# Kernel optimization log

Hardware: AMD Instinct MI355X
Metric: run time of the kernel (lower is better)

Reference implementation:

```python
import jax, jax.numpy as jnp
import numpy as np

N_GROUPS = 20000
K = 12
C_IN = 256
C_CH = 128
EPS = 1e-5


def _layernorm(x, g, b):
    mu = jnp.mean(x, axis=-1, keepdims=True)
    var = jnp.mean((x - mu) ** 2, axis=-1, keepdims=True)
    return (x - mu) * jax.lax.rsqrt(var + EPS) * g + b


def _linear(x, W, b):
    # torch nn.Linear: y = x @ W.T + b, W: [out, in]
    return x @ W.T + b


def setup_inputs() -> dict:
    key = jax.random.key(0)
    ks = jax.random.split(key, 16)
    nnz = N_GROUPS * K
    s_in = 1.0 / np.sqrt(C_IN)
    s_ch = 1.0 / np.sqrt(C_CH)
    return {
        "values": jax.random.normal(ks[0], (nnz, C_IN), jnp.float32),
        "ln_in_g": jnp.ones((C_IN,), jnp.float32),
        "ln_in_b": jnp.zeros((C_IN,), jnp.float32),
        "W_ga": jax.random.normal(ks[1], (C_CH, C_IN), jnp.float32) * s_in,
        "b_ga": jax.random.normal(ks[2], (C_CH,), jnp.float32) * 0.02,
        "W_la": jax.random.normal(ks[3], (C_CH, C_IN), jnp.float32) * s_in,
        "b_la": jnp.zeros((C_CH,), jnp.float32),
        "W_gb": jax.random.normal(ks[4], (C_CH, C_IN), jnp.float32) * s_in,
        "b_gb": jax.random.normal(ks[5], (C_CH,), jnp.float32) * 0.02,
        "W_lb": jax.random.normal(ks[6], (C_CH, C_IN), jnp.float32) * s_in,
        "b_lb": jnp.zeros((C_CH,), jnp.float32),
        "ln_o_g": jnp.ones((C_CH,), jnp.float32),
        "ln_o_b": jnp.zeros((C_CH,), jnp.float32),
        "W_go": jax.random.normal(ks[7], (C_IN, C_IN), jnp.float32) * s_in,
        "b_go": jax.random.normal(ks[8], (C_IN,), jnp.float32) * 0.02,
        "W_lo": jax.random.normal(ks[9], (C_IN, C_CH), jnp.float32) * s_ch,
        "b_lo": jax.random.normal(ks[10], (C_IN,), jnp.float32) * 0.02,
        "indices": jax.random.randint(ks[11], (4, nnz), 0, 20000, jnp.int64 if jax.config.jax_enable_x64 else jnp.int32),
    }


def reference(values, ln_in_g, ln_in_b, W_ga, b_ga, W_la, b_la, W_gb, b_gb,
              W_lb, b_lb, ln_o_g, ln_o_b, W_go, b_go, W_lo, b_lo, indices):
    nnz = values.shape[0]
    # input layer norm over channel dim of sparse values
    x = _layernorm(values, ln_in_g, ln_in_b)  # [nnz, C_IN]
    # gated projections to channel_dim
    a = jax.nn.sigmoid(_linear(x, W_ga, b_ga)) * _linear(x, W_la, b_la)  # [nnz, C_CH]
    b = jax.nn.sigmoid(_linear(x, W_gb, b_gb)) * _linear(x, W_lb, b_lb)
    a = a.reshape(nnz // K, K, C_CH)
    b = b.reshape(nnz // K, K, C_CH)
    # axis == 1: einsum('iko,jko->iko', a, b) = a * sum_j b[j]
    tri = a * jnp.sum(b, axis=0, keepdims=True)  # [nnz//K, K, C_CH]
    tri = tri.reshape(nnz, C_CH)
    # output: gate on x times linear of normed triangular update
    out = jax.nn.sigmoid(_linear(x, W_go, b_go)) * _linear(
        _layernorm(tri, ln_o_g, ln_o_b), W_lo, b_lo)  # [nnz, C_IN]
    return out
```

## Files before the change

kernel.cpp:

```cpp
#include <hip/hip_runtime.h>


#define NNZ   240000
#define ROWS  64
#define NBLK  (NNZ / ROWS)
#define PSLOTS 32

typedef __attribute__((ext_vector_type(8))) short bf16x8;
typedef __attribute__((ext_vector_type(4))) float f32x4;

__device__ __forceinline__ unsigned short f2bf(float f) {
  unsigned int u = __float_as_uint(f);
  u += 0x7fffu + ((u >> 16) & 1u);
  return (unsigned short)(u >> 16);
}
__device__ __forceinline__ float bf2f(unsigned short h) {
  return __uint_as_float(((unsigned int)h) << 16);
}

__global__ __launch_bounds__(256) void prep_kernel(
    const float* __restrict__ Wga, const float* __restrict__ Wla,
    const float* __restrict__ Wgb, const float* __restrict__ Wlb,
    const float* __restrict__ Wgo, const float* __restrict__ Wlo,
    unsigned short* __restrict__ wcat, unsigned short* __restrict__ wgo16,
    unsigned short* __restrict__ wlo16, float* __restrict__ bsum,
    float* __restrict__ bpart)
{
  const int tid = blockIdx.x * 256 + threadIdx.x;
  if (tid < 12 * 128) bsum[tid] = 0.f;
  if (tid < PSLOTS * 1536) bpart[tid] = 0.f;
  if (tid < 131072) {
    const int w8 = tid & 7, c = tid >> 3;
    const int m = c & 15, q = (c >> 4) & 3, t = (c >> 6) & 3;
    const int kb = (c >> 8) & 7, wv = c >> 11;
    const int k = kb * 32 + q * 8 + w8;
    const int ch = ((wv & 3) << 5) + ((t & 1) << 4) + m;
    const float* src = (wv < 4) ? (t < 2 ? Wga : Wla) : (t < 2 ? Wgb : Wlb);
    wcat[tid] = f2bf(src[ch * 256 + k]);
  } else if (tid < 196608) {
    const int o = tid - 131072;
    const int w8 = o & 7, c = o >> 3;
    const int m = c & 15, q = (c >> 4) & 3, nt = (c >> 6) & 1;
    const int kb = (c >> 7) & 7, wv = c >> 10;
    wgo16[o] = f2bf(Wgo[(wv * 32 + nt * 16 + m) * 256 + kb * 32 + q * 8 + w8]);
  } else if (tid < 229376) {
    const int o = tid - 196608;
    const int w8 = o & 7, c = o >> 3;
    const int m = c & 15, q = (c >> 4) & 3, nt = (c >> 6) & 1;
    const int kb = (c >> 7) & 3, wv = c >> 9;
    wlo16[o] = f2bf(Wlo[(wv * 32 + nt * 16 + m) * 128 + kb * 32 + q * 8 + w8]);
  }
}

__global__ __launch_bounds__(512, 4) void k1_kernel(
    const float* __restrict__ values,
    const float* __restrict__ ln_g, const float* __restrict__ ln_b,
    const float* __restrict__ b_ga, const float* __restrict__ b_la,
    const float* __restrict__ b_gb, const float* __restrict__ b_lb,
    const unsigned short* __restrict__ wcat,
    unsigned short* __restrict__ x_ws,
    unsigned short* __restrict__ a_ws,
    float* __restrict__ bpart)
{
  __shared__ unsigned short x_lds[ROWS][256];
  __shared__ float b_raw[ROWS][132];
  const int tid = threadIdx.x;
  const int rbase = blockIdx.x * ROWS;

  {
    const int r = tid >> 3, j = tid & 7;
    const size_t grow = (size_t)(rbase + r) * 256;
    float4 v[8];
    float s1 = 0.f, s2 = 0.f;
#pragma unroll
    for (int i = 0; i < 4; i++) {
      const int e = (j + 8 * i) * 8;
      const float4 t0 = *(const float4*)(values + grow + e);
      const float4 t1 = *(const float4*)(values + grow + e + 4);
      v[2 * i] = t0; v[2 * i + 1] = t1;
      s1 += t0.x + t0.y + t0.z + t0.w + t1.x + t1.y + t1.z + t1.w;
      s2 += t0.x * t0.x + t0.y * t0.y + t0.z * t0.z + t0.w * t0.w
          + t1.x * t1.x + t1.y * t1.y + t1.z * t1.z + t1.w * t1.w;
    }
    s1 += __shfl_xor(s1, 1); s1 += __shfl_xor(s1, 2); s1 += __shfl_xor(s1, 4);
    s2 += __shfl_xor(s2, 1); s2 += __shfl_xor(s2, 2); s2 += __shfl_xor(s2, 4);
    const float mu = s1 * (1.f / 256.f);
    const float rstd = rsqrtf(s2 * (1.f / 256.f) - mu * mu + 1e-5f);
    const int jp = j ^ (r & 7);
#pragma unroll
    for (int i = 0; i < 4; i++) {
      const int e = (j + 8 * i) * 8;
      const float4 a0 = v[2 * i], a1 = v[2 * i + 1];
      const float4 g0 = *(const float4*)(ln_g + e);
      const float4 g1 = *(const float4*)(ln_g + e + 4);
      const float4 c0 = *(const float4*)(ln_b + e);
      const float4 c1 = *(const float4*)(ln_b + e + 4);
      bf16x8 h;
      h[0] = (short)f2bf((a0.x - mu) * rstd * g0.x + c0.x);
      h[1] = (short)f2bf((a0.y - mu) * rstd * g0.y + c0.y);
      h[2] = (short)f2bf((a0.z - mu) * rstd * g0.z + c0.z);
      h[3] = (short)f2bf((a0.w - mu) * rstd * g0.w + c0.w);
      h[4] = (short)f2bf((a1.x - mu) * rstd * g1.x + c1.x);
      h[5] = (short)f2bf((a1.y - mu) * rstd * g1.y + c1.y);
      h[6] = (short)f2bf((a1.z - mu) * rstd * g1.z + c1.z);
      h[7] = (short)f2bf((a1.w - mu) * rstd * g1.w + c1.w);
      const int p = (jp + 8 * i) * 8;
      *(bf16x8*)(x_ws + grow + p) = h;
      *(bf16x8*)&x_lds[r][p] = h;
    }
  }
  __syncthreads();

  const int wv = tid >> 6;
  const int lane = tid & 63;
  const int m = lane & 15, q = lane >> 4;

  f32x4 acc[4][4];
#pragma unroll
  for (int a = 0; a < 4; a++)
#pragma unroll
    for (int b = 0; b < 4; b++) acc[a][b] = (f32x4){0.f, 0.f, 0.f, 0.f};

#pragma unroll
  for (int kb = 0; kb < 8; kb++) {
    bf16x8 A[4], B[4];
#pragma unroll
    for (int mt = 0; mt < 4; mt++)
      A[mt] = *(const bf16x8*)&x_lds[mt * 16 + m][((kb * 4 + q) ^ (m & 7)) << 3];
#pragma unroll
    for (int t = 0; t < 4; t++)
      B[t] = *(const bf16x8*)(wcat + ((((wv * 8 + kb) * 4 + t) * 64 + lane) << 3));
#pragma unroll
    for (int t = 0; t < 4; t++)
#pragma unroll
      for (int mt = 0; mt < 4; mt++)
        acc[mt][t] = __builtin_amdgcn_mfma_f32_16x16x32_bf16(A[mt], B[t], acc[mt][t], 0, 0, 0);
  }

  const bool isA = (wv < 4);
  const int chbase = (wv & 3) * 32;
  const float* bgp = isA ? b_ga : b_gb;
  const float* blp = isA ? b_la : b_lb;
#pragma unroll
  for (int t = 0; t < 2; t++) {
    const int ch = chbase + t * 16 + m;
    const float bgv = bgp[ch], blv = blp[ch];
#pragma unroll
    for (int mt = 0; mt < 4; mt++) {
#pragma unroll
      for (int rg = 0; rg < 4; rg++) {
        const int lrow = mt * 16 + q * 4 + rg;
        const float gv = acc[mt][t][rg] + bgv;
        const float lv = acc[mt][t + 2][rg] + blv;
        const float val = lv / (1.f + __expf(-gv));
        if (isA) {
          a_ws[(size_t)(rbase + lrow) * 128 + ch] = f2bf(val);
        } else {
          b_raw[lrow][ch] = val;
        }
      }
    }
  }
  __syncthreads();

  const int rb12 = rbase % 12;
  float* dst = bpart + (blockIdx.x & (PSLOTS - 1)) * 1536;
#pragma unroll
  for (int it = 0; it < 3; it++) {
    const int s = tid + it * 512;
    const int k12 = s >> 7, ch = s & 127;
    int r0 = k12 - rb12; if (r0 < 0) r0 += 12;
    float sum = 0.f;
    for (int r = r0; r < ROWS; r += 12) sum += b_raw[r][ch];
    atomicAdd(&dst[s], sum);
  }
}

__global__ __launch_bounds__(256) void reduce_kernel(
    const float* __restrict__ bpart, float* __restrict__ bsum)
{
  const int c = blockIdx.x * 256 + threadIdx.x;
  float s = 0.f;
#pragma unroll
  for (int sl = 0; sl < PSLOTS; sl++) s += bpart[sl * 1536 + c];
  bsum[c] = s;
}

__global__ __launch_bounds__(512, 4) void k2_kernel(
    const unsigned short* __restrict__ x_ws,
    const unsigned short* __restrict__ a_ws,
    const float* __restrict__ bsum,
    const float* __restrict__ ln_g, const float* __restrict__ ln_b,
    const unsigned short* __restrict__ wgo,
    const unsigned short* __restrict__ wlo,
    const float* __restrict__ b_go, const float* __restrict__ b_lo,
    float* __restrict__ out)
{
  __shared__ unsigned short x_lds[ROWS][256];
  __shared__ unsigned short t_lds[ROWS][128];
  const int tid = threadIdx.x;
  const int rbase = blockIdx.x * ROWS;

  {
    const bf16x8* xsrc = (const bf16x8*)(x_ws + (size_t)rbase * 256);
    bf16x8* xdst = (bf16x8*)&x_lds[0][0];
#pragma unroll
    for (int i = 0; i < 4; i++)
      xdst[tid + i * 512] = xsrc[tid + i * 512];

    const int r = tid >> 3, j = tid & 7;
    const int row = rbase + r;
    const int k12 = row % 12;
    const unsigned short* ar = a_ws + (size_t)row * 128;
    const float* bs = bsum + k12 * 128;
    float tv[16];
    float s1 = 0.f, s2 = 0.f;
#pragma unroll
    for (int i = 0; i < 2; i++) {
      const int e = (j + 8 * i) * 8;
      const ushort4 a0 = *(const ushort4*)(ar + e);
      const ushort4 a1 = *(const ushort4*)(ar + e + 4);
      const float4 b0 = *(const float4*)(bs + e);
      const float4 b1 = *(const float4*)(bs + e + 4);
      const float t0 = bf2f(a0.x) * b0.x, t1 = bf2f(a0.y) * b0.y;
      const float t2 = bf2f(a0.z) * b0.z, t3 = bf2f(a0.w) * b0.w;
      const float t4 = bf2f(a1.x) * b1.x, t5 = bf2f(a1.y) * b1.y;
      const float t6 = bf2f(a1.z) * b1.z, t7 = bf2f(a1.w) * b1.w;
      tv[8*i+0] = t0; tv[8*i+1] = t1; tv[8*i+2] = t2; tv[8*i+3] = t3;
      tv[8*i+4] = t4; tv[8*i+5] = t5; tv[8*i+6] = t6; tv[8*i+7] = t7;
      s1 += t0 + t1 + t2 + t3 + t4 + t5 + t6 + t7;
      s2 += t0*t0 + t1*t1 + t2*t2 + t3*t3 + t4*t4 + t5*t5 + t6*t6 + t7*t7;
    }
    s1 += __shfl_xor(s1, 1); s1 += __shfl_xor(s1, 2); s1 += __shfl_xor(s1, 4);
    s2 += __shfl_xor(s2, 1); s2 += __shfl_xor(s2, 2); s2 += __shfl_xor(s2, 4);
    const float mu = s1 * (1.f / 128.f);
    const float rstd = rsqrtf(s2 * (1.f / 128.f) - mu * mu + 1e-5f);
    const int jp = j ^ (r & 7);
#pragma unroll
    for (int i = 0; i < 2; i++) {
      const int e = (j + 8 * i) * 8;
      const float4 g0 = *(const float4*)(ln_g + e);
      const float4 g1 = *(const float4*)(ln_g + e + 4);
      const float4 c0 = *(const float4*)(ln_b + e);
      const float4 c1 = *(const float4*)(ln_b + e + 4);
      bf16x8 h;
      h[0] = (short)f2bf((tv[8*i+0] - mu) * rstd * g0.x + c0.x);
      h[1] = (short)f2bf((tv[8*i+1] - mu) * rstd * g0.y + c0.y);
      h[2] = (short)f2bf((tv[8*i+2] - mu) * rstd * g0.z + c0.z);
      h[3] = (short)f2bf((tv[8*i+3] - mu) * rstd * g0.w + c0.w);
      h[4] = (short)f2bf((tv[8*i+4] - mu) * rstd * g1.x + c1.x);
      h[5] = (short)f2bf((tv[8*i+5] - mu) * rstd * g1.y + c1.y);
      h[6] = (short)f2bf((tv[8*i+6] - mu) * rstd * g1.z + c1.z);
      h[7] = (short)f2bf((tv[8*i+7] - mu) * rstd * g1.w + c1.w);
      *(bf16x8*)&t_lds[r][(jp + 8 * i) * 8] = h;
    }
  }
  __syncthreads();

  const int wv = tid >> 6, lane = tid & 63;
  const int m = lane & 15, q = lane >> 4;

  f32x4 ag[4][2], al[4][2];
#pragma unroll
  for (int a = 0; a < 4; a++)
#pragma unroll
    for (int b = 0; b < 2; b++) { ag[a][b] = (f32x4){0.f,0.f,0.f,0.f}; al[a][b] = (f32x4){0.f,0.f,0.f,0.f}; }

#pragma unroll
  for (int kb = 0; kb < 8; kb++) {
    bf16x8 A[4], B[2];
#pragma unroll
    for (int mt = 0; mt < 4; mt++)
      A[mt] = *(const bf16x8*)&x_lds[mt * 16 + m][((kb * 4 + q) ^ (m & 7)) << 3];
#pragma unroll
    for (int nt = 0; nt < 2; nt++)
      B[nt] = *(const bf16x8*)(wgo + ((((wv * 8 + kb) * 2 + nt) * 64 + lane) << 3));
#pragma unroll
    for (int nt = 0; nt < 2; nt++)
#pragma unroll
      for (int mt = 0; mt < 4; mt++)
        ag[mt][nt] = __builtin_amdgcn_mfma_f32_16x16x32_bf16(A[mt], B[nt], ag[mt][nt], 0, 0, 0);
  }
#pragma unroll
  for (int kb = 0; kb < 4; kb++) {
    bf16x8 A[4], B[2];
#pragma unroll
    for (int mt = 0; mt < 4; mt++)
      A[mt] = *(const bf16x8*)&t_lds[mt * 16 + m][((kb * 4 + q) ^ (m & 7)) << 3];
#pragma unroll
    for (int nt = 0; nt < 2; nt++)
      B[nt] = *(const bf16x8*)(wlo + ((((wv * 4 + kb) * 2 + nt) * 64 + lane) << 3));
#pragma unroll
    for (int nt = 0; nt < 2; nt++)
#pragma unroll
      for (int mt = 0; mt < 4; mt++)
        al[mt][nt] = __builtin_amdgcn_mfma_f32_16x16x32_bf16(A[mt], B[nt], al[mt][nt], 0, 0, 0);
  }

#pragma unroll
  for (int nt = 0; nt < 2; nt++) {
    const int n = wv * 32 + nt * 16 + m;
    const float bgo = b_go[n], blo = b_lo[n];
#pragma unroll
    for (int mt = 0; mt < 4; mt++) {
#pragma unroll
      for (int rg = 0; rg < 4; rg++) {
        const int row = rbase + mt * 16 + q * 4 + rg;
        const float gv = ag[mt][nt][rg] + bgo;
        const float lv = al[mt][nt][rg] + blo;
        out[(size_t)row * 256 + n] = lv / (1.f + __expf(-gv));
      }
    }
  }
}

extern "C" void kernel_launch(void* const* d_in, const int* in_sizes, int n_in,
                              void* d_out, int out_size, void* d_ws, size_t ws_size,
                              hipStream_t stream) {
  (void)in_sizes; (void)n_in; (void)out_size; (void)ws_size;
  const float* values  = (const float*)d_in[0];
  const float* ln_in_g = (const float*)d_in[1];
  const float* ln_in_b = (const float*)d_in[2];
  const float* W_ga = (const float*)d_in[3];
  const float* b_ga = (const float*)d_in[4];
  const float* W_la = (const float*)d_in[5];
  const float* b_la = (const float*)d_in[6];
  const float* W_gb = (const float*)d_in[7];
  const float* b_gb = (const float*)d_in[8];
  const float* W_lb = (const float*)d_in[9];
  const float* b_lb = (const float*)d_in[10];
  const float* ln_o_g = (const float*)d_in[11];
  const float* ln_o_b = (const float*)d_in[12];
  const float* W_go = (const float*)d_in[13];
  const float* b_go = (const float*)d_in[14];
  const float* W_lo = (const float*)d_in[15];
  const float* b_lo = (const float*)d_in[16];

  char* ws = (char*)d_ws;
  unsigned short* x_ws  = (unsigned short*)(ws + 0);
  unsigned short* a_ws  = (unsigned short*)(ws + 122880000);
  unsigned short* wcat  = (unsigned short*)(ws + 184320000);
  unsigned short* wgo16 = (unsigned short*)(ws + 184582144);
  unsigned short* wlo16 = (unsigned short*)(ws + 184713216);
  float*          bsum  = (float*)        (ws + 184778752);
  float*          bpart = (float*)        (ws + 184784896);

  hipLaunchKernelGGL(prep_kernel, dim3(896), dim3(256), 0, stream,
                     W_ga, W_la, W_gb, W_lb, W_go, W_lo, wcat, wgo16, wlo16,
                     bsum, bpart);
  hipLaunchKernelGGL(k1_kernel, dim3(NBLK), dim3(512), 0, stream,
                     values, ln_in_g, ln_in_b, b_ga, b_la, b_gb, b_lb,
                     wcat, x_ws, a_ws, bpart);
  hipLaunchKernelGGL(reduce_kernel, dim3(6), dim3(256), 0, stream,
                     bpart, bsum);
  hipLaunchKernelGGL(k2_kernel, dim3(NBLK), dim3(512), 0, stream,
                     x_ws, a_ws, bsum, ln_o_g, ln_o_b, wgo16, wlo16, b_go, b_lo,
                     (float*)d_out);
}
```

Baseline: 627.7 us.

## Compute output gate in k1 and pass fp16 sigmoid to k2 instead of x

Moves the W_go gate GEMM and its sigmoid from k2 into k1, where the normalized x already sits in LDS. k1 writes the gate result as fp16 in an MFMA-fragment-native layout, so k2 no longer reloads x (256 bf16 per row) into LDS and only reads 256 fp16 gate values per row. k2 drops its x LDS buffer, which allows a higher occupancy hint. The gate is now stored at fp16 precision, and k1 gains extra register pressure and MFMA work.

```diff
diff --git a/kernel.cpp b/kernel.cpp
--- a/kernel.cpp
+++ b/kernel.cpp
@@ -8,6 +8,7 @@
 
 typedef __attribute__((ext_vector_type(8))) short bf16x8;
 typedef __attribute__((ext_vector_type(4))) float f32x4;
+typedef __attribute__((ext_vector_type(8))) _Float16 f16x8;
 
 __device__ __forceinline__ unsigned short f2bf(float f) {
   unsigned int u = __float_as_uint(f);
@@ -57,8 +58,10 @@
     const float* __restrict__ ln_g, const float* __restrict__ ln_b,
     const float* __restrict__ b_ga, const float* __restrict__ b_la,
     const float* __restrict__ b_gb, const float* __restrict__ b_lb,
+    const float* __restrict__ b_go,
     const unsigned short* __restrict__ wcat,
-    unsigned short* __restrict__ x_ws,
+    const unsigned short* __restrict__ wgo,
+    _Float16* __restrict__ g_ws,
     unsigned short* __restrict__ a_ws,
     float* __restrict__ bpart)
 {
@@ -104,9 +107,7 @@
       h[5] = (short)f2bf((a1.y - mu) * rstd * g1.y + c1.y);
       h[6] = (short)f2bf((a1.z - mu) * rstd * g1.z + c1.z);
       h[7] = (short)f2bf((a1.w - mu) * rstd * g1.w + c1.w);
-      const int p = (jp + 8 * i) * 8;
-      *(bf16x8*)(x_ws + grow + p) = h;
-      *(bf16x8*)&x_lds[r][p] = h;
+      *(bf16x8*)&x_lds[r][(jp + 8 * i) * 8] = h;
     }
   }
   __syncthreads();
@@ -115,51 +116,98 @@
   const int lane = tid & 63;
   const int m = lane & 15, q = lane >> 4;
 
-  f32x4 acc[4][4];
-#pragma unroll
-  for (int a = 0; a < 4; a++)
-#pragma unroll
-    for (int b = 0; b < 4; b++) acc[a][b] = (f32x4){0.f, 0.f, 0.f, 0.f};
-
-#pragma unroll
-  for (int kb = 0; kb < 8; kb++) {
-    bf16x8 A[4], B[4];
-#pragma unroll
-    for (int mt = 0; mt < 4; mt++)
-      A[mt] = *(const bf16x8*)&x_lds[mt * 16 + m][((kb * 4 + q) ^ (m & 7)) << 3];
-#pragma unroll
-    for (int t = 0; t < 4; t++)
-      B[t] = *(const bf16x8*)(wcat + ((((wv * 8 + kb) * 4 + t) * 64 + lane) << 3));
-#pragma unroll
-    for (int t = 0; t < 4; t++)
+  {
+    f32x4 acc[4][4];
+#pragma unroll
+    for (int a = 0; a < 4; a++)
+#pragma unroll
+      for (int b = 0; b < 4; b++) acc[a][b] = (f32x4){0.f, 0.f, 0.f, 0.f};
+
+#pragma unroll
+    for (int kb = 0; kb < 8; kb++) {
+      bf16x8 A[4], B[4];
 #pragma unroll
       for (int mt = 0; mt < 4; mt++)
-        acc[mt][t] = __builtin_amdgcn_mfma_f32_16x16x32_bf16(A[mt], B[t], acc[mt][t], 0, 0, 0);
-  }
-
-  const bool isA = (wv < 4);
-  const int chbase = (wv & 3) * 32;
-  const float* bgp = isA ? b_ga : b_gb;
-  const float* blp = isA ? b_la : b_lb;
-#pragma unroll
-  for (int t = 0; t < 2; t++) {
-    const int ch = chbase + t * 16 + m;
-    const float bgv = bgp[ch], blv = blp[ch];
-#pragma unroll
-    for (int mt = 0; mt < 4; mt++) {
-#pragma unroll
-      for (int rg = 0; rg < 4; rg++) {
-        const int lrow = mt * 16 + q * 4 + rg;
-        const float gv = acc[mt][t][rg] + bgv;
-        const float lv = acc[mt][t + 2][rg] + blv;
-        const float val = lv / (1.f + __expf(-gv));
-        if (isA) {
-          a_ws[(size_t)(rbase + lrow) * 128 + ch] = f2bf(val);
-        } else {
-          b_raw[lrow][ch] = val;
+        A[mt] = *(const bf16x8*)&x_lds[mt * 16 + m][((kb * 4 + q) ^ (m & 7)) << 3];
+#pragma unroll
+      for (int t = 0; t < 4; t++)
+        B[t] = *(const bf16x8*)(wcat + ((((wv * 8 + kb) * 4 + t) * 64 + lane) << 3));
+#pragma unroll
+      for (int t = 0; t < 4; t++)
+#pragma unroll
+        for (int mt = 0; mt < 4; mt++)
+          acc[mt][t] = __builtin_amdgcn_mfma_f32_16x16x32_bf16(A[mt], B[t], acc[mt][t], 0, 0, 0);
+    }
+
+    const bool isA = (wv < 4);
+    const int chbase = (wv & 3) * 32;
+    const float* bgp = isA ? b_ga : b_gb;
+    const float* blp = isA ? b_la : b_lb;
+#pragma unroll
+    for (int t = 0; t < 2; t++) {
+      const int ch = chbase + t * 16 + m;
+      const float bgv = bgp[ch], blv = blp[ch];
+#pragma unroll
+      for (int mt = 0; mt < 4; mt++) {
+#pragma unroll
+        for (int rg = 0; rg < 4; rg++) {
+          const int lrow = mt * 16 + q * 4 + rg;
+          const float gv = acc[mt][t][rg] + bgv;
+          const float lv = acc[mt][t + 2][rg] + blv;
+          const float val = lv / (1.f + __expf(-gv));
+          if (isA) {
+            a_ws[(size_t)(rbase + lrow) * 128 + ch] = f2bf(val);
+          } else {
+            b_raw[lrow][ch] = val;
+          }
         }
       }
     }
+  }
+
+  {
+    f32x4 g2[4][2];
+#pragma unroll
+    for (int a = 0; a < 4; a++)
+#pragma unroll
+      for (int b = 0; b < 2; b++) g2[a][b] = (f32x4){0.f, 0.f, 0.f, 0.f};
+
+#pragma unroll
+    for (int kb = 0; kb < 8; kb++) {
+      bf16x8 A[4], B[2];
+#pragma unroll
+      for (int mt = 0; mt < 4; mt++)
+        A[mt] = *(const bf16x8*)&x_lds[mt * 16 + m][((kb * 4 + q) ^ (m & 7)) << 3];
+#pragma unroll
+      for (int nt = 0; nt < 2; nt++)
+        B[nt] = *(const bf16x8*)(wgo + ((((wv * 8 + kb) * 2 + nt) * 64 + lane) << 3));
+#pragma unroll
+      for (int nt = 0; nt < 2; nt++)
+#pragma unroll
+        for (int mt = 0; mt < 4; mt++)
+          g2[mt][nt] = __builtin_amdgcn_mfma_f32_16x16x32_bf16(A[mt], B[nt], g2[mt][nt], 0, 0, 0);
+    }
+
+    const int n0 = wv * 32;
+    f16x8 hv[4];
+#pragma unroll
+    for (int nt = 0; nt < 2; nt++) {
+      const float bg = b_go[n0 + nt * 16 + m];
+#pragma unroll
+      for (int mt = 0; mt < 4; mt++) {
+#pragma unroll
+        for (int rg = 0; rg < 4; rg++) {
+          const float gv = g2[mt][nt][rg] + bg;
+          const float s = 1.f / (1.f + __expf(-gv));
+          const int idx = (mt * 4 + rg) * 2 + nt;
+          hv[idx >> 3][idx & 7] = (_Float16)s;
+        }
+      }
+    }
+    _Float16* gd = g_ws + ((((size_t)blockIdx.x) * 8 + wv) * 64 + lane) * 32;
+#pragma unroll
+    for (int i = 0; i < 4; i++)
+      *(f16x8*)(gd + i * 8) = hv[i];
   }
   __syncthreads();
 
@@ -186,28 +234,20 @@
   bsum[c] = s;
 }
 
-__global__ __launch_bounds__(512, 4) void k2_kernel(
-    const unsigned short* __restrict__ x_ws,
+__global__ __launch_bounds__(512, 6) void k2_kernel(
+    const _Float16* __restrict__ g_ws,
     const unsigned short* __restrict__ a_ws,
     const float* __restrict__ bsum,
     const float* __restrict__ ln_g, const float* __restrict__ ln_b,
-    const unsigned short* __restrict__ wgo,
     const unsigned short* __restrict__ wlo,
-    const float* __restrict__ b_go, const float* __restrict__ b_lo,
+    const float* __restrict__ b_lo,
     float* __restrict__ out)
 {
-  __shared__ unsigned short x_lds[ROWS][256];
   __shared__ unsigned short t_lds[ROWS][128];
   const int tid = threadIdx.x;
   const int rbase = blockIdx.x * ROWS;
 
   {
-    const bf16x8* xsrc = (const bf16x8*)(x_ws + (size_t)rbase * 256);
-    bf16x8* xdst = (bf16x8*)&x_lds[0][0];
-#pragma unroll
-    for (int i = 0; i < 4; i++)
-      xdst[tid + i * 512] = xsrc[tid + i * 512];
-
     const int r = tid >> 3, j = tid & 7;
     const int row = rbase + r;
     const int k12 = row % 12;
@@ -260,27 +300,18 @@
   const int wv = tid >> 6, lane = tid & 63;
   const int m = lane & 15, q = lane >> 4;
 
-  f32x4 ag[4][2], al[4][2];
+  const _Float16* gs = g_ws + ((((size_t)blockIdx.x) * 8 + wv) * 64 + lane) * 32;
+  f16x8 gh[4];
+#pragma unroll
+  for (int i = 0; i < 4; i++)
+    gh[i] = *(const f16x8*)(gs + i * 8);
+
+  f32x4 al[4][2];
 #pragma unroll
   for (int a = 0; a < 4; a++)
 #pragma unroll
-    for (int b = 0; b < 2; b++) { ag[a][b] = (f32x4){0.f,0.f,0.f,0.f}; al[a][b] = (f32x4){0.f,0.f,0.f,0.f}; }
-
-#pragma unroll
-  for (int kb = 0; kb < 8; kb++) {
-    bf16x8 A[4], B[2];
-#pragma unroll
-    for (int mt = 0; mt < 4; mt++)
-      A[mt] = *(const bf16x8*)&x_lds[mt * 16 + m][((kb * 4 + q) ^ (m & 7)) << 3];
-#pragma unroll
-    for (int nt = 0; nt < 2; nt++)
-      B[nt] = *(const bf16x8*)(wgo + ((((wv * 8 + kb) * 2 + nt) * 64 + lane) << 3));
-#pragma unroll
-    for (int nt = 0; nt < 2; nt++)
-#pragma unroll
-      for (int mt = 0; mt < 4; mt++)
-        ag[mt][nt] = __builtin_amdgcn_mfma_f32_16x16x32_bf16(A[mt], B[nt], ag[mt][nt], 0, 0, 0);
-  }
+    for (int b = 0; b < 2; b++) al[a][b] = (f32x4){0.f, 0.f, 0.f, 0.f};
+
 #pragma unroll
   for (int kb = 0; kb < 4; kb++) {
     bf16x8 A[4], B[2];
@@ -300,15 +331,15 @@
 #pragma unroll
   for (int nt = 0; nt < 2; nt++) {
     const int n = wv * 32 + nt * 16 + m;
-    const float bgo = b_go[n], blo = b_lo[n];
+    const float blo = b_lo[n];
 #pragma unroll
     for (int mt = 0; mt < 4; mt++) {
 #pragma unroll
       for (int rg = 0; rg < 4; rg++) {
         const int row = rbase + mt * 16 + q * 4 + rg;
-        const float gv = ag[mt][nt][rg] + bgo;
-        const float lv = al[mt][nt][rg] + blo;
-        out[(size_t)row * 256 + n] = lv / (1.f + __expf(-gv));
+        const int idx = (mt * 4 + rg) * 2 + nt;
+        const float gval = (float)gh[idx >> 3][idx & 7];
+        out[(size_t)row * 256 + n] = gval * (al[mt][nt][rg] + blo);
       }
     }
   }
@@ -337,7 +368,7 @@
   const float* b_lo = (const float*)d_in[16];
 
   char* ws = (char*)d_ws;
-  unsigned short* x_ws  = (unsigned short*)(ws + 0);
+  _Float16*       g_ws  = (_Float16*)      (ws + 0);
   unsigned short* a_ws  = (unsigned short*)(ws + 122880000);
   unsigned short* wcat  = (unsigned short*)(ws + 184320000);
   unsigned short* wgo16 = (unsigned short*)(ws + 184582144);
@@ -349,11 +380,11 @@
                      W_ga, W_la, W_gb, W_lb, W_go, W_lo, wcat, wgo16, wlo16,
                      bsum, bpart);
   hipLaunchKernelGGL(k1_kernel, dim3(NBLK), dim3(512), 0, stream,
-                     values, ln_in_g, ln_in_b, b_ga, b_la, b_gb, b_lb,
-                     wcat, x_ws, a_ws, bpart);
+                     values, ln_in_g, ln_in_b, b_ga, b_la, b_gb, b_lb, b_go,
+                     wcat, wgo16, g_ws, a_ws, bpart);
   hipLaunchKernelGGL(reduce_kernel, dim3(6), dim3(256), 0, stream,
                      bpart, bsum);
   hipLaunchKernelGGL(k2_kernel, dim3(NBLK), dim3(512), 0, stream,
-                     x_ws, a_ws, bsum, ln_o_g, ln_o_b, wgo16, wlo16, b_go, b_lo,
+                     g_ws, a_ws, bsum, ln_o_g, ln_o_b, wlo16, b_lo,
                      (float*)d_out);
 }
```

After: 662.3 us. 1.06x slower.
